# Kernel tuning notes

Measured on AMD Instinct MI355X. Metric: run time of the kernel, lower is better.

Reference implementation:

```python
import jax, jax.numpy as jnp
import numpy as np

B, T, D, H = 8, 2048, 512, 128

def setup_inputs() -> dict:
    key = jax.random.key(0)
    ks = jax.random.split(key, 8)
    s = lambda fan_in: 1.0 / np.sqrt(fan_in)
    return {
        "x": jax.random.normal(ks[0], (B, T, D), jnp.float32),
        "prediction": jax.random.normal(ks[1], (B, T, D), jnp.float32),
        "Wq": jax.random.uniform(ks[2], (D, H), jnp.float32, -s(D), s(D)),
        "bq": jnp.zeros((H,), jnp.float32),
        "Wk": jax.random.uniform(ks[3], (D, H), jnp.float32, -s(D), s(D)),
        "bk": jnp.zeros((H,), jnp.float32),
        "Wv": jax.random.uniform(ks[4], (D, D), jnp.float32, -s(D), s(D)),
        "bv": jnp.zeros((D,), jnp.float32),
        "Wf": jax.random.uniform(ks[5], (2 * D, D), jnp.float32, -s(2 * D), s(2 * D)),
        "bf": jnp.zeros((D,), jnp.float32),
    }

def reference(x, prediction, Wq, bq, Wk, bk, Wv, bv, Wf, bf):
    # q,k: [B,T,H]; v: [B,T,D]
    q = jnp.einsum('btd,dh->bth', prediction, Wq) + bq
    k = jnp.einsum('btd,dh->bth', x, Wk) + bk
    v = jnp.einsum('btd,de->bte', x, Wv) + bv
    # unscaled attention scores [B,T,T]
    scores = jnp.einsum('bth,bsh->bts', q, k)
    attn = jax.nn.softmax(scores, axis=-1)
    attended = jnp.einsum('bts,bsd->btd', attn, v)
    fusion_input = jnp.concatenate([prediction, attended], axis=-1)  # [B,T,2D]
    return jax.nn.sigmoid(jnp.einsum('btf,fd->btd', fusion_input, Wf) + bf)
```

## Files before the change

### kernel.cpp

```cpp
#include <hip/hip_runtime.h>
#include <hip/hip_bf16.h>


#define APF_B 8
#define APF_T 2048
#define APF_D 512
#define APF_H 128
#define APF_M (APF_B * APF_T)

#define GSWZ(row) ((((row) >> 1) & 3) << 3)

typedef unsigned short u16;
typedef __attribute__((ext_vector_type(8))) short short8;
typedef __attribute__((ext_vector_type(4))) float f32x4;
typedef __attribute__((ext_vector_type(16))) float f32x16;

static __device__ __forceinline__ u16 f2bf(float x) {
    union { float f; unsigned int u; } cv;
    cv.f = x;
    unsigned int u = cv.u + 0x7FFFu + ((cv.u >> 16) & 1u);
    return (u16)(u >> 16);
}
static __device__ __forceinline__ u16 f2bf_hw(float x) {
    union { __hip_bfloat16 h; u16 u; } cv;
    cv.h = __float2bfloat16(x);
    return cv.u;
}

static __device__ __forceinline__ void load16_lds(const u16* g, u16* l) {
    __builtin_amdgcn_global_load_lds(
        (const __attribute__((address_space(1))) unsigned int*)g,
        (__attribute__((address_space(3))) unsigned int*)l,
        16, 0, 0);
}

static __device__ __forceinline__ f32x16 zero16() {
    f32x16 v;
#pragma unroll
    for (int i = 0; i < 16; ++i) v[i] = 0.f;
    return v;
}

__global__ __launch_bounds__(256) void prep_w(
    const float* __restrict__ Wq, u16* __restrict__ WqT,
    const float* __restrict__ Wk, u16* __restrict__ WkT,
    const float* __restrict__ Wv, u16* __restrict__ WvT,
    const float* __restrict__ Wf, u16* __restrict__ WfT)
{
    __shared__ float tile[64][65];
    int b = blockIdx.x;
    const float* src; u16* dst; int K, N;
    if (b < 16)      { src = Wq; dst = WqT; K = 512;  N = 128; }
    else if (b < 32) { b -= 16; src = Wk; dst = WkT; K = 512;  N = 128; }
    else if (b < 96) { b -= 32; src = Wv; dst = WvT; K = 512;  N = 512; }
    else             { b -= 96; src = Wf; dst = WfT; K = 1024; N = 512; }
    const int ntN = N >> 6;
    const int k0 = (b / ntN) * 64, n0 = (b % ntN) * 64;

    const int tid = threadIdx.x;
#pragma unroll
    for (int rep = 0; rep < 4; ++rep) {
        const int r = (tid >> 4) + rep * 16;
        const int c = (tid & 15) * 4;
        const float4 v = *(const float4*)&src[(long)(k0 + r) * N + n0 + c];
        tile[r][c] = v.x; tile[r][c + 1] = v.y;
        tile[r][c + 2] = v.z; tile[r][c + 3] = v.w;
    }
    __syncthreads();
#pragma unroll
    for (int rep = 0; rep < 2; ++rep) {
        const int rn = (tid >> 3) + rep * 32;
        const int ck = (tid & 7) * 8;
        short8 o;
#pragma unroll
        for (int j = 0; j < 8; ++j)
            o[j] = (short)f2bf_hw(tile[ck + j][rn]);
        *(short8*)&dst[(long)(n0 + rn) * K + k0 + ck] = o;
    }
}

template <int ADT, int BDT, int EPI, int BIASM, int VBLK>
static __device__ __forceinline__ void gemm_body(
    u16 (&smA)[2][4096], u16 (&smB)[2][4096],
    const void* Ap, long lda,
    const void* Bp, long ldb,
    const float* bias, void* Cp, long ldc, int K,
    long row0, long col0, const float* Cadd)
{
    const int tid  = threadIdx.x;
    const int lane = tid & 63;
    const int wid  = tid >> 6;
    const int wr   = wid >> 1;
    const int wc   = wid & 1;

    f32x4 acc[4][4];
#pragma unroll
    for (int i = 0; i < 4; ++i)
#pragma unroll
        for (int j = 0; j < 4; ++j)
            acc[i][j] = (f32x4){0.f, 0.f, 0.f, 0.f};

    const int lrow = (lane >> 4) * 4;
    const int lcol = lane & 15;
    const int q8   = (lane >> 4) * 8;

    float4 ra[2][2], rb[2][2];

    auto loadA = [&](int kb) {
        if (ADT == 1) {
            const float* Af = (const float*)Ap;
#pragma unroll
            for (int rep = 0; rep < 2; ++rep) {
                const int c = tid + rep * 256;
                const int rr = c >> 2, kc = (c & 3) * 8;
                const float* ga = Af + (row0 + rr) * lda + kb + kc;
                ra[rep][0] = *(const float4*)ga;
                ra[rep][1] = *(const float4*)(ga + 4);
            }
        }
    };
    auto loadB = [&](int kb) {
        if (BDT == 1) {
            const float* Bf = (const float*)Bp;
#pragma unroll
            for (int rep = 0; rep < 2; ++rep) {
                const int c = tid + rep * 256;
                const int rr = c >> 2, kc = (c & 3) * 8;
                const float* gb = Bf + (col0 + rr) * ldb + kb + kc;
                rb[rep][0] = *(const float4*)gb;
                rb[rep][1] = *(const float4*)(gb + 4);
            }
        }
    };
    auto dmaA = [&](int buf, int kb) {
        if (ADT == 0) {
            const u16* Ab = (const u16*)Ap;
#pragma unroll
            for (int rep = 0; rep < 2; ++rep) {
                const int c = tid + rep * 256;
                const int rr = c >> 2, kc = (c & 3) * 8;
                const int wbase = (wid * 64 + rep * 256) * 8;
                load16_lds(Ab + (row0 + rr) * lda + kb + (kc ^ GSWZ(rr)),
                           &smA[buf][wbase]);
            }
        }
    };
    auto dmaB = [&](int buf, int kb) {
        if (BDT == 0) {
            const u16* Bb = (const u16*)Bp;
#pragma unroll
            for (int rep = 0; rep < 2; ++rep) {
                const int c = tid + rep * 256;
                const int rr = c >> 2, kc = (c & 3) * 8;
                const int wbase = (wid * 64 + rep * 256) * 8;
                load16_lds(Bb + (col0 + rr) * ldb + kb + (kc ^ GSWZ(rr)),
                           &smB[buf][wbase]);
            }
        }
    };
    auto cvt8 = [&](const float4& a, const float4& b) {
        short8 v;
        v[0] = (short)f2bf_hw(a.x); v[1] = (short)f2bf_hw(a.y);
        v[2] = (short)f2bf_hw(a.z); v[3] = (short)f2bf_hw(a.w);
        v[4] = (short)f2bf_hw(b.x); v[5] = (short)f2bf_hw(b.y);
        v[6] = (short)f2bf_hw(b.z); v[7] = (short)f2bf_hw(b.w);
        return v;
    };
    auto writeA = [&](int buf) {
        if (ADT == 1) {
#pragma unroll
            for (int rep = 0; rep < 2; ++rep) {
                const int c = tid + rep * 256;
                *(short8*)&smA[buf][(c * 8) ^ GSWZ(c >> 2)] =
                    cvt8(ra[rep][0], ra[rep][1]);
            }
        }
    };
    auto writeB = [&](int buf) {
        if (BDT == 1) {
#pragma unroll
            for (int rep = 0; rep < 2; ++rep) {
                const int c = tid + rep * 256;
                *(short8*)&smB[buf][(c * 8) ^ GSWZ(c >> 2)] =
                    cvt8(rb[rep][0], rb[rep][1]);
            }
        }
    };

    const int NT = K / 32;
    loadA(0); loadB(0);
    writeA(0); writeB(0);
    dmaA(0, 0); dmaB(0, 0);

    int cur = 0;
    for (int t = 0; t < NT; ++t) {
        const int kb2 = (t + 1) * 32;
        if (t + 1 < NT) { loadA(kb2); loadB(kb2); }
        __syncthreads();
        if (t + 1 < NT) { dmaA(cur ^ 1, kb2); dmaB(cur ^ 1, kb2); }

        short8 av[4], bv4[4];
#pragma unroll
        for (int ti = 0; ti < 4; ++ti) {
            const int arow = wr * 64 + ti * 16 + lcol;
            av[ti] = *(const short8*)&smA[cur][arow * 32 + (q8 ^ GSWZ(arow))];
        }
#pragma unroll
        for (int tj = 0; tj < 4; ++tj) {
            const int brow = wc * 64 + tj * 16 + lcol;
            bv4[tj] = *(const short8*)&smB[cur][brow * 32 + (q8 ^ GSWZ(brow))];
        }

#pragma unroll
        for (int ti = 0; ti < 4; ++ti)
#pragma unroll
            for (int tj = 0; tj < 4; ++tj)
                acc[ti][tj] = __builtin_amdgcn_mfma_f32_16x16x32_bf16(
                    av[ti], bv4[tj], acc[ti][tj], 0, 0, 0);

        if (t + 1 < NT) { writeA(cur ^ 1); writeB(cur ^ 1); }
        cur ^= 1;
    }

#pragma unroll
    for (int ti = 0; ti < 4; ++ti) {
        const long m0t = row0 + wr * 64 + ti * 16 + lrow;
#pragma unroll
        for (int tj = 0; tj < 4; ++tj) {
            const long n = col0 + wc * 64 + tj * 16 + lcol;
            const float bn = (BIASM == 0 && bias != nullptr) ? bias[n] : 0.f;
            if (EPI == 0) {
                u16* C = (u16*)Cp;
#pragma unroll
                for (int r = 0; r < 4; ++r) {
                    const long m = m0t + r;
                    const float bm = (BIASM == 1) ? bias[m] : bn;
                    long idx;
                    if (VBLK) {
                        idx = ((((m >> 5) * 256) + (n >> 3)) << 8) +
                              ((m & 31) << 3) + (n & 7);
                    } else {
                        idx = m * ldc + n;
                    }
                    C[idx] = f2bf(acc[ti][tj][r] + bm);
                }
            } else if (EPI == 2) {
                float* C = (float*)Cp;
#pragma unroll
                for (int r = 0; r < 4; ++r) {
                    const float val = acc[ti][tj][r] + bn;
                    C[(m0t + r) * ldc + n] = 1.0f / (1.0f + expf(-val));
                }
            } else if (EPI == 3) {
                float* C = (float*)Cp;
#pragma unroll
                for (int r = 0; r < 4; ++r)
                    C[(m0t + r) * ldc + n] = acc[ti][tj][r] + bn;
            } else {
                float* C = (float*)Cp;
#pragma unroll
                for (int r = 0; r < 4; ++r) {
                    const float val = acc[ti][tj][r] + Cadd[(m0t + r) * ldc + n];
                    C[(m0t + r) * ldc + n] = 1.0f / (1.0f + expf(-val));
                }
            }
        }
    }
}

__global__ __launch_bounds__(256, 3) void mid_gemms(
    const float* __restrict__ x, const float* __restrict__ pred,
    const u16* __restrict__ WqT, const u16* __restrict__ WkT,
    const u16* __restrict__ WvT, const u16* __restrict__ WfT,
    const float* __restrict__ bq, const float* __restrict__ bk,
    const float* __restrict__ bv, const float* __restrict__ bfu,
    u16* __restrict__ qb, u16* __restrict__ kbuf, u16* __restrict__ vTb,
    float* __restrict__ Cpre)
{
    __shared__ u16 smA[2][4096];
    __shared__ u16 smB[2][4096];

    const int bid = blockIdx.x;
    if (bid < 256) {
        const int zz = bid >> 7, by = bid & 127;
        gemm_body<1, 0, 0, 0, 0>(smA, smB,
            zz ? (const void*)x : (const void*)pred, APF_D,
            zz ? WkT : WqT, APF_D,
            zz ? bk : bq, zz ? (void*)kbuf : (void*)qb, APF_H, APF_D,
            (long)by * 128, 0, nullptr);
    } else if (bid < 768) {
        const int t = bid - 256;
        const int zz = t >> 6, rem = t & 63;
        const int bx = rem & 15, by = rem >> 4;
        gemm_body<0, 1, 0, 1, 1>(smA, smB,
            WvT, APF_D,
            (const void*)(x + (long)zz * APF_T * APF_D), APF_D,
            bv, (void*)(vTb + (long)zz * 1048576L), APF_T, APF_D,
            (long)by * 128, (long)bx * 128, nullptr);
    } else {
        const int t = bid - 768;
        const int bx = t & 3, by = t >> 2;
        gemm_body<1, 0, 3, 0, 0>(smA, smB,
            (const void*)pred, APF_D,
            WfT, 1024,
            bfu, (void*)Cpre, APF_D, APF_D,
            (long)by * 128, (long)bx * 128, nullptr);
    }
}

__global__ __launch_bounds__(256, 2) void fusion_gemm(
    const u16* __restrict__ attb, const u16* __restrict__ WfT,
    const float* __restrict__ Cpre, float* __restrict__ out)
{
    __shared__ u16 smA[2][4096];
    __shared__ u16 smB[2][4096];
    gemm_body<0, 0, 4, 0, 0>(smA, smB,
        (const void*)attb, APF_D,
        WfT + 512, 1024,
        nullptr, (void*)out, APF_D, APF_D,
        (long)blockIdx.y * 128, (long)blockIdx.x * 128, Cpre);
}

__global__ __launch_bounds__(256, 2) void attn_fused(
    const u16* __restrict__ qg, const u16* __restrict__ kg,
    const u16* __restrict__ vTg, u16* __restrict__ attg)
{
    __shared__ u16 sK[2][64 * 128];
    __shared__ u16 sP[2][64 * 64];
    __shared__ float sRS[192];

    const int tid  = threadIdx.x;
    const int lane = tid & 63;
    const int w    = tid >> 6;
    const int l31  = lane & 31;
    const int hi   = lane >> 5;
    const int qb   = w >> 1;
    const int sb   = w & 1;

    const int  bid = blockIdx.x;
    const long z   = bid & 7;
    const int  r   = bid >> 3;
    const long q0  = (long)(r & 31) * 64;
    const long d0  = (long)(r >> 5) * 256;

    const u16* kbase0 = kg + z * (long)APF_T * APF_H;

#pragma unroll
    for (int rep = 0; rep < 4; ++rep) {
        const int c    = tid + rep * 256;
        const int row  = c >> 4;
        const int col8 = (c & 15) * 8;
        load16_lds(kbase0 + row * APF_H + (col8 ^ ((row & 15) << 3)),
                   &sK[0][c * 8]);
    }

    short8 qf[8];
    {
        const u16* qsrc = qg + (z * APF_T + q0 + qb * 32 + l31) * APF_H;
#pragma unroll
        for (int ks = 0; ks < 8; ++ks)
            qf[ks] = *(const short8*)(qsrc + ks * 16 + hi * 8);
    }
    __syncthreads();

    f32x16 oacc[2][2];
#pragma unroll
    for (int i = 0; i < 2; ++i)
#pragma unroll
        for (int j = 0; j < 2; ++j) oacc[i][j] = zero16();
    f32x16 rsacc = zero16();

    const long dblk0 = (d0 >> 5) + w * 2;
    const u16* vzb = vTg + z * 1048576L + dblk0 * 65536L + (long)l31 * 8;

    const int krow = sb * 32 + l31;
    const int pcol = sb * 32 + l31;

    int cur = 0;
    for (int kt = 0; kt < APF_T / 64; ++kt) {
        f32x16 sacc = zero16();
#pragma unroll
        for (int ks = 0; ks < 8; ++ks) {
            const int colk = ks * 16 + hi * 8;
            const short8 bv =
                *(const short8*)&sK[cur][krow * 128 + (colk ^ ((krow & 15) << 3))];
            sacc = __builtin_amdgcn_mfma_f32_32x32x16_bf16(qf[ks], bv, sacc, 0, 0, 0);
        }

        if (kt + 1 < APF_T / 64) {
            const u16* ksrc = kbase0 + (long)(kt + 1) * 64 * APF_H;
#pragma unroll
            for (int rep = 0; rep < 4; ++rep) {
                const int c    = tid + rep * 256;
                const int row  = c >> 4;
                const int col8 = (c & 15) * 8;
                load16_lds(ksrc + row * APF_H + (col8 ^ ((row & 15) << 3)),
                           &sK[cur ^ 1][c * 8]);
            }
        }

        const long sbase = (long)kt * 8 + hi;
        short8 vf[2][4];
#pragma unroll
        for (int dt = 0; dt < 2; ++dt)
#pragma unroll
            for (int ks = 0; ks < 4; ++ks)
                vf[dt][ks] = *(const short8*)(vzb + dt * 65536L + (sbase + ks * 2) * 256);

#pragma unroll
        for (int rg = 0; rg < 16; ++rg) {
            const float e = __expf(sacc[rg]);
            rsacc[rg] += e;
            const int prow = qb * 32 + (rg & 3) + 8 * (rg >> 2) + 4 * hi;
            sP[cur][prow * 64 + (pcol ^ ((prow & 7) << 3))] = f2bf(e);
        }
        __syncthreads();

#pragma unroll
        for (int ks = 0; ks < 4; ++ks) {
            const int colk = ks * 16 + hi * 8;
            short8 pa[2];
#pragma unroll
            for (int qt = 0; qt < 2; ++qt) {
                const int prow = qt * 32 + l31;
                pa[qt] = *(const short8*)&sP[cur][prow * 64 + (colk ^ ((prow & 7) << 3))];
            }
#pragma unroll
            for (int dt = 0; dt < 2; ++dt)
#pragma unroll
                for (int qt = 0; qt < 2; ++qt)
                    oacc[qt][dt] = __builtin_amdgcn_mfma_f32_32x32x16_bf16(
                        pa[qt], vf[dt][ks], oacc[qt][dt], 0, 0, 0);
        }
        cur ^= 1;
    }

#pragma unroll
    for (int rg = 0; rg < 16; ++rg) {
        float s = rsacc[rg];
        s += __shfl_xor(s, 1);
        s += __shfl_xor(s, 2);
        s += __shfl_xor(s, 4);
        s += __shfl_xor(s, 8);
        s += __shfl_xor(s, 16);
        rsacc[rg] = s;
    }
    if (l31 == 0) {
#pragma unroll
        for (int rg = 0; rg < 16; ++rg) {
            const int row = (rg & 3) + 8 * (rg >> 2) + 4 * hi;
            sRS[w * 32 + row] = rsacc[rg];
        }
    }
    __syncthreads();
    if (tid < 64) {
        const int qb2 = tid >> 5, r2 = tid & 31;
        sRS[128 + tid] = 1.0f / (sRS[(qb2 * 2 + 0) * 32 + r2] +
                                 sRS[(qb2 * 2 + 1) * 32 + r2]);
    }
    __syncthreads();

    const long rowg0 = z * APF_T + q0;
    const long colg0 = d0 + (long)w * 64;
#pragma unroll
    for (int qt = 0; qt < 2; ++qt)
#pragma unroll
        for (int rg = 0; rg < 16; ++rg) {
            const int row = qt * 32 + (rg & 3) + 8 * (rg >> 2) + 4 * hi;
            const float inv = sRS[128 + row];
#pragma unroll
            for (int dt = 0; dt < 2; ++dt)
                attg[(rowg0 + row) * APF_D + colg0 + dt * 32 + l31] =
                    f2bf(oacc[qt][dt][rg] * inv);
        }
}

extern "C" void kernel_launch(void* const* d_in, const int* in_sizes, int n_in,
                              void* d_out, int out_size, void* d_ws, size_t ws_size,
                              hipStream_t stream)
{
    (void)in_sizes; (void)n_in; (void)out_size; (void)ws_size;

    const float* x    = (const float*)d_in[0];
    const float* pred = (const float*)d_in[1];
    const float* Wq   = (const float*)d_in[2];
    const float* bq   = (const float*)d_in[3];
    const float* Wk   = (const float*)d_in[4];
    const float* bk   = (const float*)d_in[5];
    const float* Wv   = (const float*)d_in[6];
    const float* bv   = (const float*)d_in[7];
    const float* Wf   = (const float*)d_in[8];
    const float* bfu  = (const float*)d_in[9];

    float* Cpre = (float*)d_ws;
    u16* wsp  = (u16*)(Cpre + (long)APF_M * APF_D);
    u16* qb   = wsp;
    u16* kbuf = qb   + (long)APF_M * APF_H;
    u16* vTb  = kbuf + (long)APF_M * APF_H;
    u16* attb = vTb  + (long)APF_M * APF_D;
    u16* WqT  = attb + (long)APF_M * APF_D;
    u16* WkT  = WqT  + (long)APF_H * APF_D;
    u16* WvT  = WkT  + (long)APF_H * APF_D;
    u16* WfT  = WvT  + (long)APF_D * APF_D;

    const dim3 thr(256);

    prep_w<<<dim3(224), thr, 0, stream>>>(Wq, WqT, Wk, WkT, Wv, WvT, Wf, WfT);

    mid_gemms<<<dim3(1280), thr, 0, stream>>>(
        x, pred, WqT, WkT, WvT, WfT, bq, bk, bv, bfu, qb, kbuf, vTb, Cpre);

    attn_fused<<<dim3(512), thr, 0, stream>>>(qb, kbuf, vTb, attb);

    fusion_gemm<<<dim3(4, 128), thr, 0, stream>>>(attb, WfT, Cpre,
                                                  (float*)d_out);
}
```

Before: 253.0 us.

## Relax barrier waits to keep prefetch loads in flight; split score MFMA chain

In the GEMM loop, the full __syncthreads is replaced by an inline s_waitcnt vmcnt(N)+s_barrier. This lets the register-prefetch global loads for the next tile stay outstanding across the barrier instead of draining them. In the attention kernel, the QK^T MFMA chain is split into two independent accumulators to break the dependency chain. The V fragment loads are moved before the K-tile DMA issue, and a manual vmcnt(0) wait is placed at the loop top. Hand-written waitcnt values depend on the exact count of outstanding loads, which risks correctness if the compiler reorders or changes how many loads are issued.

```diff
diff --git a/kernel.cpp b/kernel.cpp
--- a/kernel.cpp
+++ b/kernel.cpp
@@ -32,6 +32,16 @@
         (const __attribute__((address_space(1))) unsigned int*)g,
         (__attribute__((address_space(3))) unsigned int*)l,
         16, 0, 0);
+}
+
+template <int N>
+static __device__ __forceinline__ void bar_keep() {
+    if constexpr (N == 0)
+        asm volatile("s_waitcnt vmcnt(0) lgkmcnt(0)\ns_barrier" ::: "memory");
+    else if constexpr (N == 4)
+        asm volatile("s_waitcnt vmcnt(4) lgkmcnt(0)\ns_barrier" ::: "memory");
+    else if constexpr (N == 8)
+        asm volatile("s_waitcnt vmcnt(8) lgkmcnt(0)\ns_barrier" ::: "memory");
 }
 
 static __device__ __forceinline__ f32x16 zero16() {
@@ -187,6 +197,8 @@
         }
     };
 
+    constexpr int NREG = (ADT == 1 ? 4 : 0) + (BDT == 1 ? 4 : 0);
+
     const int NT = K / 32;
     loadA(0); loadB(0);
     writeA(0); writeB(0);
@@ -195,9 +207,13 @@
     int cur = 0;
     for (int t = 0; t < NT; ++t) {
         const int kb2 = (t + 1) * 32;
-        if (t + 1 < NT) { loadA(kb2); loadB(kb2); }
-        __syncthreads();
-        if (t + 1 < NT) { dmaA(cur ^ 1, kb2); dmaB(cur ^ 1, kb2); }
+        if (t + 1 < NT) {
+            loadA(kb2); loadB(kb2);
+            bar_keep<NREG>();
+            dmaA(cur ^ 1, kb2); dmaB(cur ^ 1, kb2);
+        } else {
+            bar_keep<0>();
+        }
 
         short8 av[4], bv4[4];
 #pragma unroll
@@ -378,14 +394,28 @@
 
     int cur = 0;
     for (int kt = 0; kt < APF_T / 64; ++kt) {
-        f32x16 sacc = zero16();
-#pragma unroll
-        for (int ks = 0; ks < 8; ++ks) {
-            const int colk = ks * 16 + hi * 8;
-            const short8 bv =
-                *(const short8*)&sK[cur][krow * 128 + (colk ^ ((krow & 15) << 3))];
-            sacc = __builtin_amdgcn_mfma_f32_32x32x16_bf16(qf[ks], bv, sacc, 0, 0, 0);
-        }
+        asm volatile("s_waitcnt vmcnt(0)" ::: "memory");
+
+        f32x16 sacc0 = zero16(), sacc1 = zero16();
+#pragma unroll
+        for (int ks = 0; ks < 4; ++ks) {
+            const int c0 = (2 * ks) * 16 + hi * 8;
+            const int c1 = (2 * ks + 1) * 16 + hi * 8;
+            const short8 bv0 =
+                *(const short8*)&sK[cur][krow * 128 + (c0 ^ ((krow & 15) << 3))];
+            const short8 bv1 =
+                *(const short8*)&sK[cur][krow * 128 + (c1 ^ ((krow & 15) << 3))];
+            sacc0 = __builtin_amdgcn_mfma_f32_32x32x16_bf16(qf[2 * ks], bv0, sacc0, 0, 0, 0);
+            sacc1 = __builtin_amdgcn_mfma_f32_32x32x16_bf16(qf[2 * ks + 1], bv1, sacc1, 0, 0, 0);
+        }
+
+        const long sbase = (long)kt * 8 + hi;
+        short8 vf[2][4];
+#pragma unroll
+        for (int dt = 0; dt < 2; ++dt)
+#pragma unroll
+            for (int ks = 0; ks < 4; ++ks)
+                vf[dt][ks] = *(const short8*)(vzb + dt * 65536L + (sbase + ks * 2) * 256);
 
         if (kt + 1 < APF_T / 64) {
             const u16* ksrc = kbase0 + (long)(kt + 1) * 64 * APF_H;
@@ -399,22 +429,14 @@
             }
         }
 
-        const long sbase = (long)kt * 8 + hi;
-        short8 vf[2][4];
-#pragma unroll
-        for (int dt = 0; dt < 2; ++dt)
-#pragma unroll
-            for (int ks = 0; ks < 4; ++ks)
-                vf[dt][ks] = *(const short8*)(vzb + dt * 65536L + (sbase + ks * 2) * 256);
-
 #pragma unroll
         for (int rg = 0; rg < 16; ++rg) {
-            const float e = __expf(sacc[rg]);
+            const float e = __expf(sacc0[rg] + sacc1[rg]);
             rsacc[rg] += e;
             const int prow = qb * 32 + (rg & 3) + 8 * (rg >> 2) + 4 * hi;
             sP[cur][prow * 64 + (pcol ^ ((prow & 7) << 3))] = f2bf(e);
         }
-        __syncthreads();
+        asm volatile("s_waitcnt lgkmcnt(0)\ns_barrier" ::: "memory");
 
 #pragma unroll
         for (int ks = 0; ks < 4; ++ks) {
```

Measured after the change: 248.9 us. No clear change (-1.6%).

## Fold Wv into fusion weight so attention writes the final sigmoid output

Applied to the files above, without the earlier changes.

Precomputes Wv·Wf_bottom (plus bias bv·Wf_bottom) so the V projection directly yields the value already mapped through the fusion weight, letting the attention kernel add Cpre and apply sigmoid in its epilogue and removing the separate fusion GEMM and the attended buffer round trip. It also replaces __syncthreads in the GEMM loop with an inline-asm barrier that waits only for older vmcnt, and switches to hardware bf16 conversion. The extra weight GEMM is tiny, but the folded weight is rounded to bf16 once more, which changes numerics slightly.

```diff
diff --git a/kernel.cpp b/kernel.cpp
--- a/kernel.cpp
+++ b/kernel.cpp
@@ -34,6 +34,16 @@
         16, 0, 0);
 }
 
+template <int N>
+static __device__ __forceinline__ void bar_keep() {
+    if constexpr (N == 0)
+        asm volatile("s_waitcnt vmcnt(0) lgkmcnt(0)\ns_barrier" ::: "memory");
+    else if constexpr (N == 4)
+        asm volatile("s_waitcnt vmcnt(4) lgkmcnt(0)\ns_barrier" ::: "memory");
+    else if constexpr (N == 8)
+        asm volatile("s_waitcnt vmcnt(8) lgkmcnt(0)\ns_barrier" ::: "memory");
+}
+
 static __device__ __forceinline__ f32x16 zero16() {
     f32x16 v;
 #pragma unroll
@@ -44,20 +54,29 @@
 __global__ __launch_bounds__(256) void prep_w(
     const float* __restrict__ Wq, u16* __restrict__ WqT,
     const float* __restrict__ Wk, u16* __restrict__ WkT,
-    const float* __restrict__ Wv, u16* __restrict__ WvT,
-    const float* __restrict__ Wf, u16* __restrict__ WfT)
+    const float* __restrict__ Wf, u16* __restrict__ WfT,
+    const float* __restrict__ bv, float* __restrict__ bvf)
 {
     __shared__ float tile[64][65];
     int b = blockIdx.x;
+    const int tid = threadIdx.x;
+
+    if (b >= 160) {
+        const int e = (b - 160) * 256 + tid;
+        float acc = 0.f;
+        for (int c = 0; c < 512; ++c)
+            acc += bv[c] * Wf[(long)(512 + c) * 512 + e];
+        bvf[e] = acc;
+        return;
+    }
+
     const float* src; u16* dst; int K, N;
     if (b < 16)      { src = Wq; dst = WqT; K = 512;  N = 128; }
     else if (b < 32) { b -= 16; src = Wk; dst = WkT; K = 512;  N = 128; }
-    else if (b < 96) { b -= 32; src = Wv; dst = WvT; K = 512;  N = 512; }
-    else             { b -= 96; src = Wf; dst = WfT; K = 1024; N = 512; }
+    else             { b -= 32; src = Wf; dst = WfT; K = 1024; N = 512; }
     const int ntN = N >> 6;
     const int k0 = (b / ntN) * 64, n0 = (b % ntN) * 64;
 
-    const int tid = threadIdx.x;
 #pragma unroll
     for (int rep = 0; rep < 4; ++rep) {
         const int r = (tid >> 4) + rep * 16;
@@ -85,7 +104,7 @@
     const void* Ap, long lda,
     const void* Bp, long ldb,
     const float* bias, void* Cp, long ldc, int K,
-    long row0, long col0, const float* Cadd)
+    long row0, long col0)
 {
     const int tid  = threadIdx.x;
     const int lane = tid & 63;
@@ -187,6 +206,8 @@
         }
     };
 
+    constexpr int NREG = (ADT == 1 ? 4 : 0) + (BDT == 1 ? 4 : 0);
+
     const int NT = K / 32;
     loadA(0); loadB(0);
     writeA(0); writeB(0);
@@ -195,9 +216,13 @@
     int cur = 0;
     for (int t = 0; t < NT; ++t) {
         const int kb2 = (t + 1) * 32;
-        if (t + 1 < NT) { loadA(kb2); loadB(kb2); }
-        __syncthreads();
-        if (t + 1 < NT) { dmaA(cur ^ 1, kb2); dmaB(cur ^ 1, kb2); }
+        if (t + 1 < NT) {
+            loadA(kb2); loadB(kb2);
+            bar_keep<NREG>();
+            dmaA(cur ^ 1, kb2); dmaB(cur ^ 1, kb2);
+        } else {
+            bar_keep<0>();
+        }
 
         short8 av[4], bv4[4];
 #pragma unroll
@@ -242,38 +267,37 @@
                     } else {
                         idx = m * ldc + n;
                     }
-                    C[idx] = f2bf(acc[ti][tj][r] + bm);
+                    C[idx] = f2bf_hw(acc[ti][tj][r] + bm);
                 }
-            } else if (EPI == 2) {
-                float* C = (float*)Cp;
-#pragma unroll
-                for (int r = 0; r < 4; ++r) {
-                    const float val = acc[ti][tj][r] + bn;
-                    C[(m0t + r) * ldc + n] = 1.0f / (1.0f + expf(-val));
-                }
-            } else if (EPI == 3) {
+            } else {
                 float* C = (float*)Cp;
 #pragma unroll
                 for (int r = 0; r < 4; ++r)
                     C[(m0t + r) * ldc + n] = acc[ti][tj][r] + bn;
-            } else {
-                float* C = (float*)Cp;
-#pragma unroll
-                for (int r = 0; r < 4; ++r) {
-                    const float val = acc[ti][tj][r] + Cadd[(m0t + r) * ldc + n];
-                    C[(m0t + r) * ldc + n] = 1.0f / (1.0f + expf(-val));
-                }
-            }
-        }
-    }
+            }
+        }
+    }
+}
+
+__global__ __launch_bounds__(256, 2) void wvf_gemm(
+    const u16* __restrict__ WfT, const float* __restrict__ Wv,
+    u16* __restrict__ WvfT)
+{
+    __shared__ u16 smA[2][4096];
+    __shared__ u16 smB[2][4096];
+    gemm_body<0, 1, 0, 0, 0>(smA, smB,
+        (const void*)(WfT + 512), 1024,
+        (const void*)Wv, APF_D,
+        nullptr, (void*)WvfT, APF_D, APF_D,
+        (long)blockIdx.y * 128, (long)blockIdx.x * 128);
 }
 
 __global__ __launch_bounds__(256, 3) void mid_gemms(
     const float* __restrict__ x, const float* __restrict__ pred,
     const u16* __restrict__ WqT, const u16* __restrict__ WkT,
-    const u16* __restrict__ WvT, const u16* __restrict__ WfT,
+    const u16* __restrict__ WvfT, const u16* __restrict__ WfT,
     const float* __restrict__ bq, const float* __restrict__ bk,
-    const float* __restrict__ bv, const float* __restrict__ bfu,
+    const float* __restrict__ bvf, const float* __restrict__ bfu,
     u16* __restrict__ qb, u16* __restrict__ kbuf, u16* __restrict__ vTb,
     float* __restrict__ Cpre)
 {
@@ -287,16 +311,16 @@
             zz ? (const void*)x : (const void*)pred, APF_D,
             zz ? WkT : WqT, APF_D,
             zz ? bk : bq, zz ? (void*)kbuf : (void*)qb, APF_H, APF_D,
-            (long)by * 128, 0, nullptr);
+            (long)by * 128, 0);
     } else if (bid < 768) {
         const int t = bid - 256;
         const int zz = t >> 6, rem = t & 63;
         const int bx = rem & 15, by = rem >> 4;
         gemm_body<0, 1, 0, 1, 1>(smA, smB,
-            WvT, APF_D,
+            WvfT, APF_D,
             (const void*)(x + (long)zz * APF_T * APF_D), APF_D,
-            bv, (void*)(vTb + (long)zz * 1048576L), APF_T, APF_D,
-            (long)by * 128, (long)bx * 128, nullptr);
+            bvf, (void*)(vTb + (long)zz * 1048576L), APF_T, APF_D,
+            (long)by * 128, (long)bx * 128);
     } else {
         const int t = bid - 768;
         const int bx = t & 3, by = t >> 2;
@@ -304,26 +328,14 @@
             (const void*)pred, APF_D,
             WfT, 1024,
             bfu, (void*)Cpre, APF_D, APF_D,
-            (long)by * 128, (long)bx * 128, nullptr);
-    }
-}
-
-__global__ __launch_bounds__(256, 2) void fusion_gemm(
-    const u16* __restrict__ attb, const u16* __restrict__ WfT,
-    const float* __restrict__ Cpre, float* __restrict__ out)
-{
-    __shared__ u16 smA[2][4096];
-    __shared__ u16 smB[2][4096];
-    gemm_body<0, 0, 4, 0, 0>(smA, smB,
-        (const void*)attb, APF_D,
-        WfT + 512, 1024,
-        nullptr, (void*)out, APF_D, APF_D,
-        (long)blockIdx.y * 128, (long)blockIdx.x * 128, Cpre);
+            (long)by * 128, (long)bx * 128);
+    }
 }
 
 __global__ __launch_bounds__(256, 2) void attn_fused(
     const u16* __restrict__ qg, const u16* __restrict__ kg,
-    const u16* __restrict__ vTg, u16* __restrict__ attg)
+    const u16* __restrict__ vTg, const float* __restrict__ Cpre,
+    float* __restrict__ outg)
 {
     __shared__ u16 sK[2][64 * 128];
     __shared__ u16 sP[2][64 * 64];
@@ -469,9 +481,11 @@
             const int row = qt * 32 + (rg & 3) + 8 * (rg >> 2) + 4 * hi;
             const float inv = sRS[128 + row];
 #pragma unroll
-            for (int dt = 0; dt < 2; ++dt)
-                attg[(rowg0 + row) * APF_D + colg0 + dt * 32 + l31] =
-                    f2bf(oacc[qt][dt][rg] * inv);
+            for (int dt = 0; dt < 2; ++dt) {
+                const long idx = (rowg0 + row) * APF_D + colg0 + dt * 32 + l31;
+                const float val = oacc[qt][dt][rg] * inv + Cpre[idx];
+                outg[idx] = 1.0f / (1.0f + expf(-val));
+            }
         }
 }
 
@@ -493,25 +507,25 @@
     const float* bfu  = (const float*)d_in[9];
 
     float* Cpre = (float*)d_ws;
-    u16* wsp  = (u16*)(Cpre + (long)APF_M * APF_D);
+    float* bvf  = Cpre + (long)APF_M * APF_D;
+    u16* wsp  = (u16*)(bvf + APF_D);
     u16* qb   = wsp;
     u16* kbuf = qb   + (long)APF_M * APF_H;
     u16* vTb  = kbuf + (long)APF_M * APF_H;
-    u16* attb = vTb  + (long)APF_M * APF_D;
-    u16* WqT  = attb + (long)APF_M * APF_D;
+    u16* WqT  = vTb  + (long)APF_M * APF_D;
     u16* WkT  = WqT  + (long)APF_H * APF_D;
-    u16* WvT  = WkT  + (long)APF_H * APF_D;
-    u16* WfT  = WvT  + (long)APF_D * APF_D;
+    u16* WfT  = WkT  + (long)APF_H * APF_D;
+    u16* WvfT = WfT  + (long)APF_D * 2 * APF_D;
 
     const dim3 thr(256);
 
-    prep_w<<<dim3(224), thr, 0, stream>>>(Wq, WqT, Wk, WkT, Wv, WvT, Wf, WfT);
+    prep_w<<<dim3(162), thr, 0, stream>>>(Wq, WqT, Wk, WkT, Wf, WfT, bv, bvf);
+
+    wvf_gemm<<<dim3(4, 4), thr, 0, stream>>>(WfT, Wv, WvfT);
 
     mid_gemms<<<dim3(1280), thr, 0, stream>>>(
-        x, pred, WqT, WkT, WvT, WfT, bq, bk, bv, bfu, qb, kbuf, vTb, Cpre);
-
-    attn_fused<<<dim3(512), thr, 0, stream>>>(qb, kbuf, vTb, attb);
-
-    fusion_gemm<<<dim3(4, 128), thr, 0, stream>>>(attb, WfT, Cpre,
-                                                  (float*)d_out);
-}
+        x, pred, WqT, WkT, WvfT, WfT, bq, bk, bvf, bfu, qb, kbuf, vTb, Cpre);
+
+    attn_fused<<<dim3(512), thr, 0, stream>>>(qb, kbuf, vTb, Cpre,
+                                              (float*)d_out);
+}
```

Measured after the change: 276.1 us. 1.09x slower.

## Relax GEMM barrier waits and remap blocks for XCD-local reuse

Applied to the files above, without the earlier changes.

Replaces __syncthreads in the GEMM main loop with an inline s_waitcnt/s_barrier that waits only for older loads (vmcnt of N). In-flight register prefetches can then stay outstanding across the barrier while the LDS DMA loads complete. Remaps block indices in the V-projection and Cpre GEMMs so consecutive block IDs, which land on different XCDs, share data within an XCD for better L2 reuse. Also switches the bf16 conversion to the hardware intrinsic and drops the unused EPI==2 branch. The hand-tuned vmcnt values carry a correctness risk if the compiler reorders or changes the number of outstanding loads.

```diff
diff --git a/kernel.cpp b/kernel.cpp
--- a/kernel.cpp
+++ b/kernel.cpp
@@ -32,6 +32,16 @@
         (const __attribute__((address_space(1))) unsigned int*)g,
         (__attribute__((address_space(3))) unsigned int*)l,
         16, 0, 0);
+}
+
+template <int N>
+static __device__ __forceinline__ void bar_keep() {
+    if constexpr (N == 0)
+        asm volatile("s_waitcnt vmcnt(0) lgkmcnt(0)\ns_barrier" ::: "memory");
+    else if constexpr (N == 4)
+        asm volatile("s_waitcnt vmcnt(4) lgkmcnt(0)\ns_barrier" ::: "memory");
+    else if constexpr (N == 8)
+        asm volatile("s_waitcnt vmcnt(8) lgkmcnt(0)\ns_barrier" ::: "memory");
 }
 
 static __device__ __forceinline__ f32x16 zero16() {
@@ -187,6 +197,8 @@
         }
     };
 
+    constexpr int NREG = (ADT == 1 ? 4 : 0) + (BDT == 1 ? 4 : 0);
+
     const int NT = K / 32;
     loadA(0); loadB(0);
     writeA(0); writeB(0);
@@ -195,9 +207,13 @@
     int cur = 0;
     for (int t = 0; t < NT; ++t) {
         const int kb2 = (t + 1) * 32;
-        if (t + 1 < NT) { loadA(kb2); loadB(kb2); }
-        __syncthreads();
-        if (t + 1 < NT) { dmaA(cur ^ 1, kb2); dmaB(cur ^ 1, kb2); }
+        if (t + 1 < NT) {
+            loadA(kb2); loadB(kb2);
+            bar_keep<NREG>();
+            dmaA(cur ^ 1, kb2); dmaB(cur ^ 1, kb2);
+        } else {
+            bar_keep<0>();
+        }
 
         short8 av[4], bv4[4];
 #pragma unroll
@@ -242,14 +258,7 @@
                     } else {
                         idx = m * ldc + n;
                     }
-                    C[idx] = f2bf(acc[ti][tj][r] + bm);
-                }
-            } else if (EPI == 2) {
-                float* C = (float*)Cp;
-#pragma unroll
-                for (int r = 0; r < 4; ++r) {
-                    const float val = acc[ti][tj][r] + bn;
-                    C[(m0t + r) * ldc + n] = 1.0f / (1.0f + expf(-val));
+                    C[idx] = f2bf_hw(acc[ti][tj][r] + bm);
                 }
             } else if (EPI == 3) {
                 float* C = (float*)Cp;
@@ -290,8 +299,9 @@
             (long)by * 128, 0, nullptr);
     } else if (bid < 768) {
         const int t = bid - 256;
-        const int zz = t >> 6, rem = t & 63;
-        const int bx = rem & 15, by = rem >> 4;
+        const int zz = t & 7;
+        const int idx = t >> 3;
+        const int bx = idx & 15, by = idx >> 4;
         gemm_body<0, 1, 0, 1, 1>(smA, smB,
             WvT, APF_D,
             (const void*)(x + (long)zz * APF_T * APF_D), APF_D,
@@ -299,7 +309,9 @@
             (long)by * 128, (long)bx * 128, nullptr);
     } else {
         const int t = bid - 768;
-        const int bx = t & 3, by = t >> 2;
+        const int xcd = t & 7, j = t >> 3;
+        const int by = xcd + 8 * (j >> 2);
+        const int bx = j & 3;
         gemm_body<1, 0, 3, 0, 0>(smA, smB,
             (const void*)pred, APF_D,
             WfT, 1024,
```

After: 242.6 us. 4.1% less time.
